# Kernel tuning notes

Hardware: AMD Instinct MI355X
Metric: run time of the kernel (lower is better)

The kernel has to match this reference:

```python
import jax, jax.numpy as jnp
import numpy as np

DIM = 1024
N_HEADS = 16
N_KV = 4
HEAD_DIM = 64
HIDDEN = 2048
N_EXP = 8
TOP_K = 2
B, T = 2, 1024
EPS = 1e-6


def rmsnorm(x, w):
    rms = jnp.sqrt(jnp.mean(x * x, axis=-1, keepdims=True) + EPS)
    return w * x / rms


def apply_rope(x, cos, sin):
    # x: [B, H, T, D]; cos/sin: [T, D//2]
    Tn = x.shape[2]
    c = cos[None, None, :Tn, :]
    s = sin[None, None, :Tn, :]
    xe = x[..., 0::2]
    xo = x[..., 1::2]
    re = xe * c - xo * s
    ro = xe * s + xo * c
    return jnp.stack([re, ro], axis=-1).reshape(x.shape)


def setup_inputs() -> dict:
    key = jax.random.key(0)
    ks = jax.random.split(key, 12)
    sd = DIM ** -0.5
    x = jax.random.normal(ks[0], (B, T, DIM), dtype=jnp.float32)
    # RoPE tables
    half = HEAD_DIM // 2
    inv_freq = 1.0 / (10000.0 ** (np.arange(0, half, dtype=np.float32) / half))
    pos = np.arange(T, dtype=np.float32)
    ang = np.outer(pos, inv_freq)
    cos = jnp.asarray(np.cos(ang), dtype=jnp.float32)
    sin = jnp.asarray(np.sin(ang), dtype=jnp.float32)
    return {
        "x": x,
        "cos": cos,
        "sin": sin,
        "norm_attn_w": jnp.ones((DIM,), jnp.float32),
        "wq": jax.random.normal(ks[1], (N_HEADS * HEAD_DIM, DIM), jnp.float32) * sd,
        "wk": jax.random.normal(ks[2], (N_KV * HEAD_DIM, DIM), jnp.float32) * sd,
        "wv": jax.random.normal(ks[3], (N_KV * HEAD_DIM, DIM), jnp.float32) * sd,
        "wo": jax.random.normal(ks[4], (DIM, N_HEADS * HEAD_DIM), jnp.float32) * sd,
        "norm_ffn_w": jnp.ones((DIM,), jnp.float32),
        "router_w": jax.random.normal(ks[5], (N_EXP, DIM), jnp.float32) * sd,
        "router_b": jnp.zeros((N_EXP,), jnp.float32),
        "w_gate": jax.random.normal(ks[6], (N_EXP, HIDDEN, DIM), jnp.float32) * sd,
        "w_up": jax.random.normal(ks[7], (N_EXP, HIDDEN, DIM), jnp.float32) * sd,
        "w_down": jax.random.normal(ks[8], (N_EXP, DIM, HIDDEN), jnp.float32) * (HIDDEN ** -0.5),
    }


def attention(x, cos, sin, wq, wk, wv, wo):
    Bn, Tn, _ = x.shape
    q = (x @ wq.T).reshape(Bn, Tn, N_HEADS, HEAD_DIM).transpose(0, 2, 1, 3)
    k = (x @ wk.T).reshape(Bn, Tn, N_KV, HEAD_DIM).transpose(0, 2, 1, 3)
    v = (x @ wv.T).reshape(Bn, Tn, N_KV, HEAD_DIM).transpose(0, 2, 1, 3)
    q = apply_rope(q, cos, sin)
    k = apply_rope(k, cos, sin)
    rep = N_HEADS // N_KV
    k = jnp.repeat(k, rep, axis=1)
    v = jnp.repeat(v, rep, axis=1)
    scale = HEAD_DIM ** -0.5
    scores = jnp.einsum("bhqd,bhkd->bhqk", q, k) * scale
    causal = jnp.triu(jnp.ones((Tn, Tn), dtype=bool), k=1)
    scores = jnp.where(causal[None, None], -jnp.inf, scores)
    attn = jax.nn.softmax(scores, axis=-1)
    out = jnp.einsum("bhqk,bhkd->bhqd", attn, v)
    out = out.transpose(0, 2, 1, 3).reshape(Bn, Tn, N_HEADS * HEAD_DIM)
    return out @ wo.T


def moe(x, router_w, router_b, w_gate, w_up, w_down):
    Bn, Tn, D = x.shape
    flat = x.reshape(-1, D)  # [N, D]
    N = flat.shape[0]
    logits = flat @ router_w.T + router_b
    probs = jax.nn.softmax(logits, axis=-1)
    top_vals, top_idx = jax.lax.top_k(probs, TOP_K)
    top_vals = top_vals / (jnp.sum(top_vals, axis=-1, keepdims=True) + 1e-9)
    # combine weights [N, E]
    comb = jnp.zeros((N, N_EXP), flat.dtype).at[jnp.arange(N)[:, None], top_idx].add(top_vals)
    g = jnp.einsum("nd,ehd->enh", flat, w_gate)
    u = jnp.einsum("nd,ehd->enh", flat, w_up)
    h = jax.nn.silu(g) * u
    eo = jnp.einsum("enh,edh->end", h, w_down)  # [E, N, D]
    out = jnp.einsum("ne,end->nd", comb, eo)
    return out.reshape(Bn, Tn, D)


def reference(x, cos, sin, norm_attn_w, wq, wk, wv, wo, norm_ffn_w, router_w, router_b, w_gate, w_up, w_down):
    x = x + attention(rmsnorm(x, norm_attn_w), cos, sin, wq, wk, wv, wo)
    x = x + moe(rmsnorm(x, norm_ffn_w), router_w, router_b, w_gate, w_up, w_down)
    return x
```

## Files before the change

### kernel.cpp

```cpp
#include <hip/hip_runtime.h>
#include <math.h>

#define N_TOK   2048
#define SEQ     1024
#define DIMM    1024
#define NH      16
#define NKV     4
#define HD      64
#define HID     2048
#define NEXP    8
#define QKVW    1536

typedef __attribute__((ext_vector_type(4))) float f32x4;
typedef __attribute__((ext_vector_type(8))) short s16x8;
typedef unsigned short u16;

__device__ __forceinline__ u16 f2bf(float f) {
    union { float f; unsigned u; } v; v.f = f;
    unsigned r = v.u + 0x7fffu + ((v.u >> 16) & 1u);
    return (u16)(r >> 16);
}
__device__ __forceinline__ float bf2f(u16 h) {
    union { unsigned u; float f; } v; v.u = ((unsigned)h) << 16;
    return v.f;
}

__device__ __forceinline__ f32x4 mfma16(s16x8 a, s16x8 b, f32x4 c) {
    return __builtin_amdgcn_mfma_f32_16x16x32_bf16(a, b, c, 0, 0, 0);
}

__device__ __forceinline__ int lds_byte(int row, int byte_in_row, int swz_key) {
    return row * 128 + (byte_in_row ^ ((swz_key & 7) << 4));
}

__device__ __forceinline__ s16x8 ldfrag(const char* base, int row, int ks, int lane) {
    int b = lds_byte(row, ks * 64 + ((lane >> 4) * 16), row);
    return *(const s16x8*)(base + b);
}

__device__ __forceinline__ void gload16(const void* g, void* l) {
    __builtin_amdgcn_global_load_lds(
        (const __attribute__((address_space(1))) void*)g,
        (__attribute__((address_space(3))) void*)l, 16, 0, 0);
}

__global__ __launch_bounds__(256) void cvt_all(const float* __restrict__ wq,
    const float* __restrict__ wk, const float* __restrict__ wv, const float* __restrict__ wo,
    u16* __restrict__ hi, u16* __restrict__ lo,
    const float* __restrict__ a, const float* __restrict__ b, const float* __restrict__ c,
    u16* __restrict__ oa, u16* __restrict__ ob, u16* __restrict__ oc)
{
    if (blockIdx.x < 1024) {
        int i = blockIdx.x * 256 + threadIdx.x;
        int stride = 1024 * 256;
        for (; i < 655360; i += stride) {
            const float* in; int j;
            if (i < 262144)      { in = wq; j = i; }
            else if (i < 327680) { in = wk; j = i - 262144; }
            else if (i < 393216) { in = wv; j = i - 327680; }
            else                 { in = wo; j = i - 393216; }
            f32x4 v = __builtin_nontemporal_load((const f32x4*)in + j);
            ushort4 h, l;
            h.x = f2bf(v[0]); h.y = f2bf(v[1]); h.z = f2bf(v[2]); h.w = f2bf(v[3]);
            l.x = f2bf(v[0] - bf2f(h.x)); l.y = f2bf(v[1] - bf2f(h.y));
            l.z = f2bf(v[2] - bf2f(h.z)); l.w = f2bf(v[3] - bf2f(h.w));
            reinterpret_cast<ushort4*>(hi)[i] = h;
            reinterpret_cast<ushort4*>(lo)[i] = l;
        }
    } else {
        const int n4 = 4 << 20;
        int i = ((blockIdx.x - 1024) * 256 + threadIdx.x) * 2;
        int stride = 3072 * 256 * 2;
        for (; i < 3 * n4; i += stride) {
            int seg = i >> 22, j = i & (n4 - 1);
            const f32x4* in = (const f32x4*)((seg == 0) ? a : (seg == 1) ? b : c);
            ushort4* out = (ushort4*)((seg == 0) ? oa : (seg == 1) ? ob : oc);
            f32x4 v0 = __builtin_nontemporal_load(in + j);
            f32x4 v1 = __builtin_nontemporal_load(in + j + 1);
            ushort4 o0, o1;
            o0.x = f2bf(v0[0]); o0.y = f2bf(v0[1]); o0.z = f2bf(v0[2]); o0.w = f2bf(v0[3]);
            o1.x = f2bf(v1[0]); o1.y = f2bf(v1[1]); o1.z = f2bf(v1[2]); o1.w = f2bf(v1[3]);
            out[j] = o0;
            out[j + 1] = o1;
        }
    }
}

__global__ __launch_bounds__(256) void rmsnorm_split(const float* __restrict__ x,
    const float* __restrict__ w, u16* __restrict__ oh, u16* __restrict__ ol)
{
    int row = blockIdx.x;
    const float4* xr = reinterpret_cast<const float4*>(x + (size_t)row * DIMM);
    const float4* wr = reinterpret_cast<const float4*>(w);
    float4 v = xr[threadIdx.x];
    float ss = v.x*v.x + v.y*v.y + v.z*v.z + v.w*v.w;
#pragma unroll
    for (int off = 32; off; off >>= 1) ss += __shfl_xor(ss, off);
    __shared__ float red[4];
    int wid = threadIdx.x >> 6, lane = threadIdx.x & 63;
    if (lane == 0) red[wid] = ss;
    __syncthreads();
    float tot = red[0] + red[1] + red[2] + red[3];
    float inv = rsqrtf(tot * (1.0f/DIMM) + 1e-6f);
    float4 ww = wr[threadIdx.x];
    float4 o;
    o.x = ww.x * v.x * inv;
    o.y = ww.y * v.y * inv;
    o.z = ww.z * v.z * inv;
    o.w = ww.w * v.w * inv;
    ushort4 h, l;
    h.x = f2bf(o.x); h.y = f2bf(o.y); h.z = f2bf(o.z); h.w = f2bf(o.w);
    l.x = f2bf(o.x - bf2f(h.x)); l.y = f2bf(o.y - bf2f(h.y));
    l.z = f2bf(o.z - bf2f(h.z)); l.w = f2bf(o.w - bf2f(h.w));
    reinterpret_cast<ushort4*>(oh + (size_t)row * DIMM)[threadIdx.x] = h;
    reinterpret_cast<ushort4*>(ol + (size_t)row * DIMM)[threadIdx.x] = l;
}

__global__ __launch_bounds__(256) void rmsnorm_router(const float* __restrict__ x,
    const float* __restrict__ w, const float* __restrict__ rw, const float* __restrict__ rb,
    u16* __restrict__ outb, float* __restrict__ logits)
{
    int row = blockIdx.x;
    int tid = threadIdx.x;
    int wid = tid >> 6, lane = tid & 63;
    const float4* xr = reinterpret_cast<const float4*>(x + (size_t)row * DIMM);
    const float4* wr = reinterpret_cast<const float4*>(w);
    float4 v = xr[tid];
    float ss = v.x*v.x + v.y*v.y + v.z*v.z + v.w*v.w;
#pragma unroll
    for (int off = 32; off; off >>= 1) ss += __shfl_xor(ss, off);
    __shared__ float red[4];
    __shared__ float lred[4][NEXP];
    if (lane == 0) red[wid] = ss;
    __syncthreads();
    float tot = red[0] + red[1] + red[2] + red[3];
    float inv = rsqrtf(tot * (1.0f/DIMM) + 1e-6f);
    float4 ww = wr[tid];
    float4 o;
    o.x = ww.x * v.x * inv;
    o.y = ww.y * v.y * inv;
    o.z = ww.z * v.z * inv;
    o.w = ww.w * v.w * inv;
    ushort4 ob;
    ob.x = f2bf(o.x); ob.y = f2bf(o.y); ob.z = f2bf(o.z); ob.w = f2bf(o.w);
    reinterpret_cast<ushort4*>(outb + (size_t)row * DIMM)[tid] = ob;
    float acc[NEXP];
#pragma unroll
    for (int e = 0; e < NEXP; e++) {
        float4 r4 = reinterpret_cast<const float4*>(rw + (size_t)e * DIMM)[tid];
        acc[e] = o.x * r4.x + o.y * r4.y + o.z * r4.z + o.w * r4.w;
    }
#pragma unroll
    for (int e = 0; e < NEXP; e++) {
        float p = acc[e];
#pragma unroll
        for (int off = 32; off; off >>= 1) p += __shfl_xor(p, off);
        acc[e] = p;
    }
    if (lane == 0)
#pragma unroll
        for (int e = 0; e < NEXP; e++) lred[wid][e] = acc[e];
    __syncthreads();
    if (tid < NEXP)
        logits[(size_t)row * NEXP + tid] =
            lred[0][tid] + lred[1][tid] + lred[2][tid] + lred[3][tid] + rb[tid];
}

__global__ __launch_bounds__(256) void top2_kernel(const float* __restrict__ logits,
    int* __restrict__ top_idx, float* __restrict__ top_w)
{
    int n = blockIdx.x * 256 + threadIdx.x;
    if (n >= N_TOK) return;
    float lg[NEXP];
#pragma unroll
    for (int e = 0; e < NEXP; e++) lg[e] = logits[(size_t)n * NEXP + e];
    float m = lg[0];
#pragma unroll
    for (int e = 1; e < NEXP; e++) m = fmaxf(m, lg[e]);
    float pe[NEXP], s = 0.f;
#pragma unroll
    for (int e = 0; e < NEXP; e++) { pe[e] = __expf(lg[e] - m); s += pe[e]; }
    int i1 = 0; float v1 = pe[0];
#pragma unroll
    for (int e = 1; e < NEXP; e++) if (pe[e] > v1) { v1 = pe[e]; i1 = e; }
    int i2 = -1; float v2 = -1.f;
#pragma unroll
    for (int e = 0; e < NEXP; e++) if (e != i1 && pe[e] > v2) { v2 = pe[e]; i2 = e; }
    v1 /= s; v2 /= s;
    float den = v1 + v2 + 1e-9f;
    top_idx[2 * n] = i1; top_idx[2 * n + 1] = i2;
    top_w[2 * n] = v1 / den; top_w[2 * n + 1] = v2 / den;
}

__global__ __launch_bounds__(256) void route_build(const int* __restrict__ top_idx,
    const float* __restrict__ top_w, int* __restrict__ counts, int* __restrict__ offs,
    int* __restrict__ assign_token, float* __restrict__ assign_w)
{
    __shared__ int lcnt[NEXP], loff[NEXP], lpos[NEXP];
    int tid = threadIdx.x;
    if (tid < NEXP) { lcnt[tid] = 0; lpos[tid] = 0; }
    __syncthreads();
    for (int i = tid; i < 2 * N_TOK; i += 256)
        atomicAdd(&lcnt[top_idx[i]], 1);
    __syncthreads();
    if (tid == 0) {
        int s = 0;
        for (int e = 0; e < NEXP; e++) { loff[e] = s; s += lcnt[e]; }
    }
    __syncthreads();
    if (tid < NEXP) { counts[tid] = lcnt[tid]; offs[tid] = loff[tid]; }
    for (int i = tid; i < 2 * N_TOK; i += 256) {
        int e = top_idx[i];
        int p = atomicAdd(&lpos[e], 1);
        int r = loff[e] + p;
        assign_token[r] = i >> 1;
        assign_w[r] = top_w[i];
    }
}

__global__ __launch_bounds__(256) void gemm_bs(const u16* __restrict__ Ah_,
    const u16* __restrict__ Al_, const u16* __restrict__ Bh_, const u16* __restrict__ Bl_,
    float* __restrict__ C, const float* __restrict__ R, int M, int N, int K, int ldc)
{
    __shared__ __align__(16) u16 Ah[128 * 64], Al[128 * 64];
    __shared__ __align__(16) u16 Bh[64 * 64],  Bl[64 * 64];
    int tid = threadIdx.x;
    int m0 = blockIdx.y * 128, n0 = blockIdx.x * 64;
    int lane = tid & 63, wv = tid >> 6;
    int wm = wv >> 1, wn = wv & 1;
    int sr = lane >> 3, sc = lane & 7;

    f32x4 acc[4][2];
#pragma unroll
    for (int i = 0; i < 4; i++)
#pragma unroll
        for (int j = 0; j < 2; j++) acc[i][j] = f32x4{0.f, 0.f, 0.f, 0.f};

    const int NT = K >> 6;
    int bid = blockIdx.x + gridDim.x * blockIdx.y;
    int ph = (bid * 5) & (NT - 1);

    for (int tt = 0; tt < NT; ++tt) {
        int k0 = ((tt + ph) & (NT - 1)) << 6;
#pragma unroll
        for (int i = 0; i < 4; i++) {
            int row = wv * 32 + i * 8 + sr;
            int c = sc ^ (row & 7);
            size_t g = (size_t)(m0 + row) * K + k0 + c * 8;
            gload16(Ah_ + g, (void*)(Ah + (wv * 4 + i) * 512));
            gload16(Al_ + g, (void*)(Al + (wv * 4 + i) * 512));
        }
#pragma unroll
        for (int i = 0; i < 2; i++) {
            int row = wv * 16 + i * 8 + sr;
            int c = sc ^ (row & 7);
            size_t g = (size_t)(n0 + row) * K + k0 + c * 8;
            gload16(Bh_ + g, (void*)(Bh + (wv * 2 + i) * 512));
            gload16(Bl_ + g, (void*)(Bl + (wv * 2 + i) * 512));
        }
        __syncthreads();
#pragma unroll
        for (int ks = 0; ks < 2; ++ks) {
            s16x8 afh[4], afl[4], bfh[2], bfl[2];
#pragma unroll
            for (int mi = 0; mi < 4; mi++) {
                int row = wm * 64 + mi * 16 + (lane & 15);
                afh[mi] = ldfrag((const char*)Ah, row, ks, lane);
                afl[mi] = ldfrag((const char*)Al, row, ks, lane);
            }
#pragma unroll
            for (int nj = 0; nj < 2; nj++) {
                int row = wn * 32 + nj * 16 + (lane & 15);
                bfh[nj] = ldfrag((const char*)Bh, row, ks, lane);
                bfl[nj] = ldfrag((const char*)Bl, row, ks, lane);
            }
#pragma unroll
            for (int mi = 0; mi < 4; mi++)
#pragma unroll
                for (int nj = 0; nj < 2; nj++) {
                    acc[mi][nj] = mfma16(afl[mi], bfh[nj], acc[mi][nj]);
                    acc[mi][nj] = mfma16(afh[mi], bfl[nj], acc[mi][nj]);
                    acc[mi][nj] = mfma16(afh[mi], bfh[nj], acc[mi][nj]);
                }
        }
        __syncthreads();
    }
#pragma unroll
    for (int mi = 0; mi < 4; mi++)
#pragma unroll
        for (int nj = 0; nj < 2; nj++)
#pragma unroll
            for (int r = 0; r < 4; r++) {
                int m = m0 + wm * 64 + mi * 16 + (lane >> 4) * 4 + r;
                int n = n0 + wn * 32 + nj * 16 + (lane & 15);
                float v = acc[mi][nj][r];
                if (R) v += R[(size_t)m * ldc + n];
                C[(size_t)m * ldc + n] = v;
            }
}

__global__ __launch_bounds__(256) void rope_both(const float* __restrict__ qkvb,
    const float* __restrict__ cs, const float* __restrict__ sn,
    u16* __restrict__ qsh, u16* __restrict__ qsl,
    u16* __restrict__ ksh, u16* __restrict__ ksl)
{
    int gid = blockIdx.x * 256 + threadIdx.x;
    const int QTOT = N_TOK * NH * 32;
    const int KTOT = N_TOK * NKV * 32;
    int nheads, base_col, out_w;
    u16 *oh, *ol;
    if (gid < QTOT) {
        nheads = NH; base_col = 0; out_w = NH * HD; oh = qsh; ol = qsl;
    } else {
        gid -= QTOT;
        if (gid >= KTOT) return;
        nheads = NKV; base_col = 1024; out_w = NKV * HD; oh = ksh; ol = ksl;
    }
    int i = gid & 31;
    int h = (gid >> 5) % nheads;
    int n = gid / (32 * nheads);
    int t = n & (SEQ - 1);
    const float* p = qkvb + (size_t)n * QKVW + base_col + h * HD + 2 * i;
    float xe = p[0], xo = p[1];
    float c = cs[t * 32 + i], s = sn[t * 32 + i];
    float re = xe * c - xo * s;
    float ro = xe * s + xo * c;
    size_t o = (size_t)n * out_w + h * HD + 2 * i;
    u16 reh = f2bf(re), roh = f2bf(ro);
    oh[o] = reh;     oh[o + 1] = roh;
    ol[o] = f2bf(re - bf2f(reh));
    ol[o + 1] = f2bf(ro - bf2f(roh));
}

__global__ __launch_bounds__(256) void transpose_v_split(const float* __restrict__ qkvb,
    u16* __restrict__ vth, u16* __restrict__ vtl)
{
    __shared__ float t[64][65];
    int bx = blockIdx.x;
    int by = blockIdx.y;
    int tid = threadIdx.x;
    int c4 = tid & 15, r0 = tid >> 4;
#pragma unroll
    for (int i = 0; i < 4; i++) {
        int row = r0 + i * 16;
        float4 vv = *(const float4*)(qkvb + (size_t)(bx * 64 + row) * QKVW + 1280 + by * 64 + c4 * 4);
        t[c4 * 4 + 0][row] = vv.x;
        t[c4 * 4 + 1][row] = vv.y;
        t[c4 * 4 + 2][row] = vv.z;
        t[c4 * 4 + 3][row] = vv.w;
    }
    __syncthreads();
#pragma unroll
    for (int i = 0; i < 4; i++) {
        int drow = r0 + i * 16;
        ushort4 hh, ll;
        float a = t[drow][c4 * 4 + 0], b = t[drow][c4 * 4 + 1];
        float c = t[drow][c4 * 4 + 2], d = t[drow][c4 * 4 + 3];
        hh.x = f2bf(a); hh.y = f2bf(b); hh.z = f2bf(c); hh.w = f2bf(d);
        ll.x = f2bf(a - bf2f(hh.x)); ll.y = f2bf(b - bf2f(hh.y));
        ll.z = f2bf(c - bf2f(hh.z)); ll.w = f2bf(d - bf2f(hh.w));
        size_t o = ((size_t)(by * 64 + drow) * N_TOK + bx * 64 + c4 * 4) >> 2;
        reinterpret_cast<ushort4*>(vth)[o] = hh;
        reinterpret_cast<ushort4*>(vtl)[o] = ll;
    }
}

__global__ __launch_bounds__(256) void attn_mfma(const u16* __restrict__ qsh,
    const u16* __restrict__ qsl, const u16* __restrict__ ksh, const u16* __restrict__ ksl,
    const u16* __restrict__ vth, const u16* __restrict__ vtl,
    u16* __restrict__ outh, u16* __restrict__ outl)
{
    int b = blockIdx.z, h = blockIdx.y;
    int qt = (gridDim.x - 1) - blockIdx.x;
    int kvh = h >> 2;
    int tid = threadIdx.x;
    int lane = tid & 63, wv = tid >> 6;
    int q0 = qt * 64;
    int sr = lane >> 3, sc = lane & 7;

    __shared__ __align__(16) u16 Qh[64 * 64], Ql[64 * 64];
    __shared__ __align__(16) u16 Kh[64 * 64], Kl[64 * 64];
    __shared__ __align__(16) u16 Vh[64 * 64], Vl[64 * 64];
    __shared__ __align__(16) char Ph[4][16 * 128], Pl[4][16 * 128];

#pragma unroll
    for (int i = 0; i < 2; i++) {
        int row = wv * 16 + i * 8 + sr;
        int c = sc ^ (row & 7);
        size_t g = (size_t)(b * SEQ + q0 + row) * (NH * HD) + h * HD + c * 8;
        gload16(qsh + g, (void*)(Qh + (wv * 2 + i) * 512));
        gload16(qsl + g, (void*)(Ql + (wv * 2 + i) * 512));
    }
    __syncthreads();

    s16x8 aQh[2], aQl[2];
#pragma unroll
    for (int ks = 0; ks < 2; ks++) {
        aQh[ks] = ldfrag((const char*)Qh, wv * 16 + (lane & 15), ks, lane);
        aQl[ks] = ldfrag((const char*)Ql, wv * 16 + (lane & 15), ks, lane);
    }

    float m_run[4], l_run[4];
    f32x4 acc_o[4];
#pragma unroll
    for (int r = 0; r < 4; r++) { m_run[r] = -1e30f; l_run[r] = 0.f; }
#pragma unroll
    for (int nj = 0; nj < 4; nj++) acc_o[nj] = f32x4{0.f, 0.f, 0.f, 0.f};

    for (int kt = 0; kt <= qt; kt++) {
        int kbase = kt * 64;
        __syncthreads();
#pragma unroll
        for (int i = 0; i < 2; i++) {
            int row = wv * 16 + i * 8 + sr;
            int c = sc ^ (row & 7);
            size_t gk = (size_t)(b * SEQ + kbase + row) * (NKV * HD) + kvh * HD + c * 8;
            size_t gv = (size_t)(kvh * HD + row) * N_TOK + b * SEQ + kbase + c * 8;
            gload16(ksh + gk, (void*)(Kh + (wv * 2 + i) * 512));
            gload16(ksl + gk, (void*)(Kl + (wv * 2 + i) * 512));
            gload16(vth + gv, (void*)(Vh + (wv * 2 + i) * 512));
            gload16(vtl + gv, (void*)(Vl + (wv * 2 + i) * 512));
        }
        __syncthreads();

        f32x4 sacc[4];
#pragma unroll
        for (int nj = 0; nj < 4; nj++) sacc[nj] = f32x4{0.f, 0.f, 0.f, 0.f};
#pragma unroll
        for (int ks = 0; ks < 2; ks++) {
#pragma unroll
            for (int nj = 0; nj < 4; nj++) {
                s16x8 bKh = ldfrag((const char*)Kh, nj * 16 + (lane & 15), ks, lane);
                s16x8 bKl = ldfrag((const char*)Kl, nj * 16 + (lane & 15), ks, lane);
                sacc[nj] = mfma16(aQl[ks], bKh, sacc[nj]);
                sacc[nj] = mfma16(aQh[ks], bKl, sacc[nj]);
                sacc[nj] = mfma16(aQh[ks], bKh, sacc[nj]);
            }
        }

        float sv[4][4];
#pragma unroll
        for (int nj = 0; nj < 4; nj++)
#pragma unroll
            for (int r = 0; r < 4; r++) {
                float s = sacc[nj][r] * 0.125f;
                if (kt == qt) {
                    int row_loc = wv * 16 + (lane >> 4) * 4 + r;
                    int col_loc = nj * 16 + (lane & 15);
                    if (col_loc > row_loc) s = -1e30f;
                }
                sv[nj][r] = s;
            }

        float p[4][4];
#pragma unroll
        for (int r = 0; r < 4; r++) {
            float mx = fmaxf(fmaxf(sv[0][r], sv[1][r]), fmaxf(sv[2][r], sv[3][r]));
            mx = fmaxf(mx, __shfl_xor(mx, 1));
            mx = fmaxf(mx, __shfl_xor(mx, 2));
            mx = fmaxf(mx, __shfl_xor(mx, 4));
            mx = fmaxf(mx, __shfl_xor(mx, 8));
            float m_new = fmaxf(m_run[r], mx);
            float corr = __expf(m_run[r] - m_new);
            float ps = 0.f;
#pragma unroll
            for (int nj = 0; nj < 4; nj++) {
                float pv = __expf(sv[nj][r] - m_new);
                p[nj][r] = pv;
                ps += pv;
            }
            ps += __shfl_xor(ps, 1);
            ps += __shfl_xor(ps, 2);
            ps += __shfl_xor(ps, 4);
            ps += __shfl_xor(ps, 8);
            l_run[r] = l_run[r] * corr + ps;
            m_run[r] = m_new;
#pragma unroll
            for (int nj = 0; nj < 4; nj++) acc_o[nj][r] *= corr;
        }

        char* phb = Ph[wv];
        char* plb = Pl[wv];
#pragma unroll
        for (int nj = 0; nj < 4; nj++)
#pragma unroll
            for (int r = 0; r < 4; r++) {
                int row = (lane >> 4) * 4 + r;
                int col = nj * 16 + (lane & 15);
                u16 hh = f2bf(p[nj][r]);
                u16 ll = f2bf(p[nj][r] - bf2f(hh));
                int byte = lds_byte(row, col * 2, row);
                *(u16*)(phb + byte) = hh;
                *(u16*)(plb + byte) = ll;
            }

#pragma unroll
        for (int ks = 0; ks < 2; ks++) {
            s16x8 aPh = ldfrag(phb, lane & 15, ks, lane);
            s16x8 aPl = ldfrag(plb, lane & 15, ks, lane);
#pragma unroll
            for (int nj = 0; nj < 4; nj++) {
                s16x8 bVh = ldfrag((const char*)Vh, nj * 16 + (lane & 15), ks, lane);
                s16x8 bVl = ldfrag((const char*)Vl, nj * 16 + (lane & 15), ks, lane);
                acc_o[nj] = mfma16(aPl, bVh, acc_o[nj]);
                acc_o[nj] = mfma16(aPh, bVl, acc_o[nj]);
                acc_o[nj] = mfma16(aPh, bVh, acc_o[nj]);
            }
        }
    }

#pragma unroll
    for (int r = 0; r < 4; r++) {
        int row_glob = q0 + wv * 16 + (lane >> 4) * 4 + r;
        float inv = 1.f / l_run[r];
#pragma unroll
        for (int nj = 0; nj < 4; nj++) {
            int dv = nj * 16 + (lane & 15);
            size_t idx = (size_t)(b * SEQ + row_glob) * (NH * HD) + h * HD + dv;
            float v = acc_o[nj][r] * inv;
            u16 hh = f2bf(v);
            outh[idx] = hh;
            outl[idx] = f2bf(v - bf2f(hh));
        }
    }
}

__global__ __launch_bounds__(256) void moe_gateup2(const u16* __restrict__ xb,
    const u16* __restrict__ wgb, const u16* __restrict__ wub,
    const int* __restrict__ assign_token, const int* __restrict__ offs,
    const int* __restrict__ counts, u16* __restrict__ hbufb)
{
    int e = blockIdx.z;
    int cnt = counts[e];
    int t0 = blockIdx.y * 128;
    if (t0 >= cnt) return;
    int base = offs[e];
    int h0 = blockIdx.x * 64;
    __shared__ __align__(16) u16 As[128 * 64];
    __shared__ __align__(16) u16 Gs[64 * 64];
    __shared__ __align__(16) u16 Us[64 * 64];
    __shared__ int toks[128];
    int tid = threadIdx.x;
    if (tid < 128) {
        int a = t0 + tid;
        toks[tid] = (a < cnt) ? assign_token[base + a] : 0;
    }
    __syncthreads();
    int lane = tid & 63, wv = tid >> 6;
    int wm = wv >> 1, wn = wv & 1;
    int sr = lane >> 3, sc = lane & 7;

    int tokr[4];
#pragma unroll
    for (int i = 0; i < 4; i++) tokr[i] = toks[wv * 32 + i * 8 + sr];

    const u16* wge = wgb + (size_t)e * HID * DIMM;
    const u16* wue = wub + (size_t)e * HID * DIMM;

    f32x4 accg[4][2], accu[4][2];
#pragma unroll
    for (int i = 0; i < 4; i++)
#pragma unroll
        for (int j = 0; j < 2; j++) { accg[i][j] = f32x4{0,0,0,0}; accu[i][j] = f32x4{0,0,0,0}; }

    const int NT = DIMM / 64;
    int bid = blockIdx.x + gridDim.x * (blockIdx.y + gridDim.y * blockIdx.z);
    int ph = (bid * 5) & (NT - 1);

    for (int tt = 0; tt < NT; ++tt) {
        int k0 = ((tt + ph) & (NT - 1)) << 6;
#pragma unroll
        for (int i = 0; i < 4; i++) {
            int row = wv * 32 + i * 8 + sr;
            int c = sc ^ (row & 7);
            gload16(xb + (size_t)tokr[i] * DIMM + k0 + c * 8, (void*)(As + (wv * 4 + i) * 512));
        }
#pragma unroll
        for (int i = 0; i < 2; i++) {
            int row = wv * 16 + i * 8 + sr;
            int c = sc ^ (row & 7);
            gload16(wge + (size_t)(h0 + row) * DIMM + k0 + c * 8, (void*)(Gs + (wv * 2 + i) * 512));
            gload16(wue + (size_t)(h0 + row) * DIMM + k0 + c * 8, (void*)(Us + (wv * 2 + i) * 512));
        }
        __syncthreads();
#pragma unroll
        for (int ks = 0; ks < 2; ++ks) {
            s16x8 af[4], gf[2], uf[2];
#pragma unroll
            for (int mi = 0; mi < 4; mi++)
                af[mi] = ldfrag((const char*)As, wm * 64 + mi * 16 + (lane & 15), ks, lane);
#pragma unroll
            for (int nj = 0; nj < 2; nj++) {
                int row = wn * 32 + nj * 16 + (lane & 15);
                gf[nj] = ldfrag((const char*)Gs, row, ks, lane);
                uf[nj] = ldfrag((const char*)Us, row, ks, lane);
            }
#pragma unroll
            for (int mi = 0; mi < 4; mi++)
#pragma unroll
                for (int nj = 0; nj < 2; nj++) {
                    accg[mi][nj] = mfma16(af[mi], gf[nj], accg[mi][nj]);
                    accu[mi][nj] = mfma16(af[mi], uf[nj], accu[mi][nj]);
                }
        }
        __syncthreads();
    }
#pragma unroll
    for (int mi = 0; mi < 4; mi++)
#pragma unroll
        for (int nj = 0; nj < 2; nj++)
#pragma unroll
            for (int r = 0; r < 4; r++) {
                int row = wm * 64 + mi * 16 + (lane >> 4) * 4 + r;
                if (t0 + row < cnt) {
                    int col = wn * 32 + nj * 16 + (lane & 15);
                    float g = accg[mi][nj][r], u = accu[mi][nj][r];
                    float hh = (g / (1.f + __expf(-g))) * u;
                    hbufb[(size_t)(base + t0 + row) * HID + h0 + col] = f2bf(hh);
                }
            }
}

__global__ __launch_bounds__(256) void moe_down2(const u16* __restrict__ hbufb,
    const u16* __restrict__ wdb, const int* __restrict__ assign_token,
    const float* __restrict__ assign_w, const int* __restrict__ offs,
    const int* __restrict__ counts, float* __restrict__ out)
{
    int e = blockIdx.z;
    int cnt = counts[e];
    int t0 = blockIdx.y * 128;
    if (t0 >= cnt) return;
    int base = offs[e];
    int d0 = blockIdx.x * 128;
    __shared__ __align__(16) u16 As[128 * 64];
    __shared__ __align__(16) u16 Bs[128 * 64];
    __shared__ int toks[128];
    __shared__ float rw_[128];
    int tid = threadIdx.x;
    if (tid < 128) {
        int a = t0 + tid;
        toks[tid] = (a < cnt) ? assign_token[base + a] : 0;
        rw_[tid] = (a < cnt) ? assign_w[base + a] : 0.f;
    }
    __syncthreads();
    int lane = tid & 63, wv = tid >> 6;
    int wm = wv >> 1, wn = wv & 1;
    int sr = lane >> 3, sc = lane & 7;

    const u16* wde = wdb + (size_t)e * DIMM * HID;

    f32x4 acc[4][4];
#pragma unroll
    for (int i = 0; i < 4; i++)
#pragma unroll
        for (int j = 0; j < 4; j++) acc[i][j] = f32x4{0,0,0,0};

    const int NT = HID / 64;
    int bid = blockIdx.x + gridDim.x * (blockIdx.y + gridDim.y * blockIdx.z);
    int ph = (bid * 5) & (NT - 1);

    for (int tt = 0; tt < NT; ++tt) {
        int k0 = ((tt + ph) & (NT - 1)) << 6;
#pragma unroll
        for (int i = 0; i < 4; i++) {
            int row = wv * 32 + i * 8 + sr;
            int c = sc ^ (row & 7);
            gload16(hbufb + (size_t)(base + t0 + row) * HID + k0 + c * 8, (void*)(As + (wv * 4 + i) * 512));
            gload16(wde + (size_t)(d0 + row) * HID + k0 + c * 8, (void*)(Bs + (wv * 4 + i) * 512));
        }
        __syncthreads();
#pragma unroll
        for (int ks = 0; ks < 2; ++ks) {
            s16x8 af[4];
#pragma unroll
            for (int mi = 0; mi < 4; mi++)
                af[mi] = ldfrag((const char*)As, wm * 64 + mi * 16 + (lane & 15), ks, lane);
#pragma unroll
            for (int nj = 0; nj < 4; nj++) {
                s16x8 bf = ldfrag((const char*)Bs, wn * 64 + nj * 16 + (lane & 15), ks, lane);
#pragma unroll
                for (int mi = 0; mi < 4; mi++)
                    acc[mi][nj] = mfma16(af[mi], bf, acc[mi][nj]);
            }
        }
        __syncthreads();
    }
#pragma unroll
    for (int mi = 0; mi < 4; mi++)
#pragma unroll
        for (int r = 0; r < 4; r++) {
            int row = wm * 64 + mi * 16 + (lane >> 4) * 4 + r;
            if (t0 + row < cnt) {
                int tok = toks[row];
                float w = rw_[row];
#pragma unroll
                for (int nj = 0; nj < 4; nj++) {
                    int col = d0 + wn * 64 + nj * 16 + (lane & 15);
                    atomicAdd(&out[(size_t)tok * DIMM + col], acc[mi][nj][r] * w);
                }
            }
        }
}

extern "C" void kernel_launch(void* const* d_in, const int* in_sizes, int n_in,
                              void* d_out, int out_size, void* d_ws, size_t ws_size,
                              hipStream_t stream)
{
    const float* x      = (const float*)d_in[0];
    const float* cs     = (const float*)d_in[1];
    const float* sn     = (const float*)d_in[2];
    const float* w_na   = (const float*)d_in[3];
    const float* wq     = (const float*)d_in[4];
    const float* wk     = (const float*)d_in[5];
    const float* wv     = (const float*)d_in[6];
    const float* wo     = (const float*)d_in[7];
    const float* w_nf   = (const float*)d_in[8];
    const float* rw     = (const float*)d_in[9];
    const float* rb     = (const float*)d_in[10];
    const float* wg     = (const float*)d_in[11];
    const float* wu     = (const float*)d_in[12];
    const float* wd     = (const float*)d_in[13];
    float* out = (float*)d_out;

    const size_t F = 1024 * 1024;
    float* wsf = (float*)d_ws;

    float* qkvb = wsf;
    float* tail = wsf + 3 * F;
    u16* qsh    = (u16*)(wsf + 3 * F + F / 2);
    u16* qsl    = (u16*)(wsf + 4 * F + F / 2);
    u16* ksh    = (u16*)(wsf + 5 * F + F / 2);
    u16* ksl    = (u16*)(wsf + 5 * F + 3 * F / 4);
    u16* vth    = (u16*)(wsf + 6 * F);
    u16* vtl    = (u16*)(wsf + 6 * F + F / 4);
    u16* xn2b   = (u16*)(wsf + 6 * F + F / 2);
    u16* hbufb  = (u16*)(wsf + 7 * F + F / 2);
    u16* xnh    = (u16*)(wsf + 7 * F + F / 2);
    u16* xnl    = (u16*)(wsf + 8 * F + F / 2);
    u16* attnh  = (u16*)(wsf + 9 * F + F / 2);
    u16* attnl  = (u16*)(wsf + 10 * F + F / 2);
    u16* wgb    = (u16*)(wsf + 11 * F + F / 2);
    u16* wub    = (u16*)(wsf + 19 * F + F / 2);
    u16* wdb    = (u16*)(wsf + 27 * F + F / 2);
    u16* wqkvoh = (u16*)(wsf + 35 * F + F / 2);
    u16* wqkvol = (u16*)(wsf + 36 * F + 3 * F / 4);

    int*   top_idx      = (int*)tail;
    float* top_w        = tail + 4096;
    int*   counts       = (int*)(tail + 8192);
    int*   offs         = (int*)(tail + 8192) + 8;
    int*   assign_token = (int*)(tail + 8192) + 32;
    float* assign_w     = tail + 8192 + 32 + 4096;
    float* logits       = tail + 8192 + 32 + 8192;

    cvt_all<<<4096, 256, 0, stream>>>(wq, wk, wv, wo, wqkvoh, wqkvol,
                                      wg, wu, wd, wgb, wub, wdb);
    rmsnorm_split<<<N_TOK, 256, 0, stream>>>(x, w_na, xnh, xnl);
    gemm_bs<<<dim3(QKVW / 64, 16), 256, 0, stream>>>(xnh, xnl, wqkvoh, wqkvol,
                                                     qkvb, nullptr, N_TOK, QKVW, DIMM, QKVW);
    rope_both<<<(N_TOK * (NH + NKV) * 32 + 255) / 256, 256, 0, stream>>>(qkvb, cs, sn, qsh, qsl, ksh, ksl);
    transpose_v_split<<<dim3(N_TOK / 64, (NKV * HD) / 64), 256, 0, stream>>>(qkvb, vth, vtl);
    attn_mfma<<<dim3(SEQ / 64, NH, 2), 256, 0, stream>>>(qsh, qsl, ksh, ksl, vth, vtl, attnh, attnl);
    gemm_bs<<<dim3(DIMM / 64, 16), 256, 0, stream>>>(attnh, attnl,
                                                     wqkvoh + (size_t)1536 * 1024, wqkvol + (size_t)1536 * 1024,
                                                     out, x, N_TOK, DIMM, NH * HD, DIMM);
    rmsnorm_router<<<N_TOK, 256, 0, stream>>>(out, w_nf, rw, rb, xn2b, logits);
    top2_kernel<<<N_TOK / 256, 256, 0, stream>>>(logits, top_idx, top_w);
    route_build<<<1, 256, 0, stream>>>(top_idx, top_w, counts, offs, assign_token, assign_w);
    moe_gateup2<<<dim3(HID / 64, 16, NEXP), 256, 0, stream>>>(xn2b, wgb, wub, assign_token, offs, counts, hbufb);
    moe_down2<<<dim3(DIMM / 128, 16, NEXP), 256, 0, stream>>>(hbufb, wdb, assign_token, assign_w, offs, counts, out);
}
```

Baseline: 332.4 us.

## Merge small kernels and overlap MoE weight conversion with attention

```diff
diff --git a/kernel.cpp b/kernel.cpp
--- a/kernel.cpp
+++ b/kernel.cpp
@@ -44,11 +44,11 @@
         (__attribute__((address_space(3))) void*)l, 16, 0, 0);
 }
 
-__global__ __launch_bounds__(256) void cvt_all(const float* __restrict__ wq,
+__global__ __launch_bounds__(256) void prep1(const float* __restrict__ wq,
     const float* __restrict__ wk, const float* __restrict__ wv, const float* __restrict__ wo,
     u16* __restrict__ hi, u16* __restrict__ lo,
-    const float* __restrict__ a, const float* __restrict__ b, const float* __restrict__ c,
-    u16* __restrict__ oa, u16* __restrict__ ob, u16* __restrict__ oc)
+    const float* __restrict__ x, const float* __restrict__ w_na,
+    u16* __restrict__ oh, u16* __restrict__ ol)
 {
     if (blockIdx.x < 1024) {
         int i = blockIdx.x * 256 + threadIdx.x;
@@ -68,57 +68,37 @@
             reinterpret_cast<ushort4*>(lo)[i] = l;
         }
     } else {
-        const int n4 = 4 << 20;
-        int i = ((blockIdx.x - 1024) * 256 + threadIdx.x) * 2;
-        int stride = 3072 * 256 * 2;
-        for (; i < 3 * n4; i += stride) {
-            int seg = i >> 22, j = i & (n4 - 1);
-            const f32x4* in = (const f32x4*)((seg == 0) ? a : (seg == 1) ? b : c);
-            ushort4* out = (ushort4*)((seg == 0) ? oa : (seg == 1) ? ob : oc);
-            f32x4 v0 = __builtin_nontemporal_load(in + j);
-            f32x4 v1 = __builtin_nontemporal_load(in + j + 1);
-            ushort4 o0, o1;
-            o0.x = f2bf(v0[0]); o0.y = f2bf(v0[1]); o0.z = f2bf(v0[2]); o0.w = f2bf(v0[3]);
-            o1.x = f2bf(v1[0]); o1.y = f2bf(v1[1]); o1.z = f2bf(v1[2]); o1.w = f2bf(v1[3]);
-            out[j] = o0;
-            out[j + 1] = o1;
-        }
-    }
-}
-
-__global__ __launch_bounds__(256) void rmsnorm_split(const float* __restrict__ x,
-    const float* __restrict__ w, u16* __restrict__ oh, u16* __restrict__ ol)
-{
-    int row = blockIdx.x;
-    const float4* xr = reinterpret_cast<const float4*>(x + (size_t)row * DIMM);
-    const float4* wr = reinterpret_cast<const float4*>(w);
-    float4 v = xr[threadIdx.x];
-    float ss = v.x*v.x + v.y*v.y + v.z*v.z + v.w*v.w;
-#pragma unroll
-    for (int off = 32; off; off >>= 1) ss += __shfl_xor(ss, off);
-    __shared__ float red[4];
-    int wid = threadIdx.x >> 6, lane = threadIdx.x & 63;
-    if (lane == 0) red[wid] = ss;
-    __syncthreads();
-    float tot = red[0] + red[1] + red[2] + red[3];
-    float inv = rsqrtf(tot * (1.0f/DIMM) + 1e-6f);
-    float4 ww = wr[threadIdx.x];
-    float4 o;
-    o.x = ww.x * v.x * inv;
-    o.y = ww.y * v.y * inv;
-    o.z = ww.z * v.z * inv;
-    o.w = ww.w * v.w * inv;
-    ushort4 h, l;
-    h.x = f2bf(o.x); h.y = f2bf(o.y); h.z = f2bf(o.z); h.w = f2bf(o.w);
-    l.x = f2bf(o.x - bf2f(h.x)); l.y = f2bf(o.y - bf2f(h.y));
-    l.z = f2bf(o.z - bf2f(h.z)); l.w = f2bf(o.w - bf2f(h.w));
-    reinterpret_cast<ushort4*>(oh + (size_t)row * DIMM)[threadIdx.x] = h;
-    reinterpret_cast<ushort4*>(ol + (size_t)row * DIMM)[threadIdx.x] = l;
+        int row = blockIdx.x - 1024;
+        const float4* xr = reinterpret_cast<const float4*>(x + (size_t)row * DIMM);
+        const float4* wr = reinterpret_cast<const float4*>(w_na);
+        float4 v = xr[threadIdx.x];
+        float ss = v.x*v.x + v.y*v.y + v.z*v.z + v.w*v.w;
+#pragma unroll
+        for (int off = 32; off; off >>= 1) ss += __shfl_xor(ss, off);
+        __shared__ float red[4];
+        int wid = threadIdx.x >> 6, lane = threadIdx.x & 63;
+        if (lane == 0) red[wid] = ss;
+        __syncthreads();
+        float tot = red[0] + red[1] + red[2] + red[3];
+        float inv = rsqrtf(tot * (1.0f/DIMM) + 1e-6f);
+        float4 ww = wr[threadIdx.x];
+        float4 o;
+        o.x = ww.x * v.x * inv;
+        o.y = ww.y * v.y * inv;
+        o.z = ww.z * v.z * inv;
+        o.w = ww.w * v.w * inv;
+        ushort4 h, l;
+        h.x = f2bf(o.x); h.y = f2bf(o.y); h.z = f2bf(o.z); h.w = f2bf(o.w);
+        l.x = f2bf(o.x - bf2f(h.x)); l.y = f2bf(o.y - bf2f(h.y));
+        l.z = f2bf(o.z - bf2f(h.z)); l.w = f2bf(o.w - bf2f(h.w));
+        reinterpret_cast<ushort4*>(oh + (size_t)row * DIMM)[threadIdx.x] = h;
+        reinterpret_cast<ushort4*>(ol + (size_t)row * DIMM)[threadIdx.x] = l;
+    }
 }
 
 __global__ __launch_bounds__(256) void rmsnorm_router(const float* __restrict__ x,
     const float* __restrict__ w, const float* __restrict__ rw, const float* __restrict__ rb,
-    u16* __restrict__ outb, float* __restrict__ logits)
+    u16* __restrict__ outb, int* __restrict__ top_idx, float* __restrict__ top_w)
 {
     int row = blockIdx.x;
     int tid = threadIdx.x;
@@ -161,35 +141,28 @@
 #pragma unroll
         for (int e = 0; e < NEXP; e++) lred[wid][e] = acc[e];
     __syncthreads();
-    if (tid < NEXP)
-        logits[(size_t)row * NEXP + tid] =
-            lred[0][tid] + lred[1][tid] + lred[2][tid] + lred[3][tid] + rb[tid];
-}
-
-__global__ __launch_bounds__(256) void top2_kernel(const float* __restrict__ logits,
-    int* __restrict__ top_idx, float* __restrict__ top_w)
-{
-    int n = blockIdx.x * 256 + threadIdx.x;
-    if (n >= N_TOK) return;
-    float lg[NEXP];
-#pragma unroll
-    for (int e = 0; e < NEXP; e++) lg[e] = logits[(size_t)n * NEXP + e];
-    float m = lg[0];
-#pragma unroll
-    for (int e = 1; e < NEXP; e++) m = fmaxf(m, lg[e]);
-    float pe[NEXP], s = 0.f;
-#pragma unroll
-    for (int e = 0; e < NEXP; e++) { pe[e] = __expf(lg[e] - m); s += pe[e]; }
-    int i1 = 0; float v1 = pe[0];
-#pragma unroll
-    for (int e = 1; e < NEXP; e++) if (pe[e] > v1) { v1 = pe[e]; i1 = e; }
-    int i2 = -1; float v2 = -1.f;
-#pragma unroll
-    for (int e = 0; e < NEXP; e++) if (e != i1 && pe[e] > v2) { v2 = pe[e]; i2 = e; }
-    v1 /= s; v2 /= s;
-    float den = v1 + v2 + 1e-9f;
-    top_idx[2 * n] = i1; top_idx[2 * n + 1] = i2;
-    top_w[2 * n] = v1 / den; top_w[2 * n + 1] = v2 / den;
+    if (tid == 0) {
+        float lg[NEXP];
+#pragma unroll
+        for (int e = 0; e < NEXP; e++)
+            lg[e] = lred[0][e] + lred[1][e] + lred[2][e] + lred[3][e] + rb[e];
+        float m = lg[0];
+#pragma unroll
+        for (int e = 1; e < NEXP; e++) m = fmaxf(m, lg[e]);
+        float pe[NEXP], s = 0.f;
+#pragma unroll
+        for (int e = 0; e < NEXP; e++) { pe[e] = __expf(lg[e] - m); s += pe[e]; }
+        int i1 = 0; float v1 = pe[0];
+#pragma unroll
+        for (int e = 1; e < NEXP; e++) if (pe[e] > v1) { v1 = pe[e]; i1 = e; }
+        int i2 = -1; float v2 = -1.f;
+#pragma unroll
+        for (int e = 0; e < NEXP; e++) if (e != i1 && pe[e] > v2) { v2 = pe[e]; i2 = e; }
+        v1 /= s; v2 /= s;
+        float den = v1 + v2 + 1e-9f;
+        top_idx[2 * row] = i1; top_idx[2 * row + 1] = i2;
+        top_w[2 * row] = v1 / den; top_w[2 * row + 1] = v2 / den;
+    }
 }
 
 __global__ __launch_bounds__(256) void route_build(const int* __restrict__ top_idx,
@@ -299,79 +272,100 @@
             }
 }
 
-__global__ __launch_bounds__(256) void rope_both(const float* __restrict__ qkvb,
+__global__ __launch_bounds__(256) void prep2(const float* __restrict__ qkvb,
     const float* __restrict__ cs, const float* __restrict__ sn,
     u16* __restrict__ qsh, u16* __restrict__ qsl,
-    u16* __restrict__ ksh, u16* __restrict__ ksl)
-{
-    int gid = blockIdx.x * 256 + threadIdx.x;
-    const int QTOT = N_TOK * NH * 32;
-    const int KTOT = N_TOK * NKV * 32;
-    int nheads, base_col, out_w;
-    u16 *oh, *ol;
-    if (gid < QTOT) {
-        nheads = NH; base_col = 0; out_w = NH * HD; oh = qsh; ol = qsl;
+    u16* __restrict__ ksh, u16* __restrict__ ksl,
+    u16* __restrict__ vth, u16* __restrict__ vtl)
+{
+    const int ROPE_BLOCKS = (N_TOK * (NH + NKV) * 32) / 256;
+    if (blockIdx.x < ROPE_BLOCKS) {
+        int gid = blockIdx.x * 256 + threadIdx.x;
+        const int QTOT = N_TOK * NH * 32;
+        int nheads, base_col, out_w;
+        u16 *oh, *ol;
+        if (gid < QTOT) {
+            nheads = NH; base_col = 0; out_w = NH * HD; oh = qsh; ol = qsl;
+        } else {
+            gid -= QTOT;
+            nheads = NKV; base_col = 1024; out_w = NKV * HD; oh = ksh; ol = ksl;
+        }
+        int i = gid & 31;
+        int h = (gid >> 5) % nheads;
+        int n = gid / (32 * nheads);
+        int t = n & (SEQ - 1);
+        const float* p = qkvb + (size_t)n * QKVW + base_col + h * HD + 2 * i;
+        float xe = p[0], xo = p[1];
+        float c = cs[t * 32 + i], s = sn[t * 32 + i];
+        float re = xe * c - xo * s;
+        float ro = xe * s + xo * c;
+        size_t o = (size_t)n * out_w + h * HD + 2 * i;
+        u16 reh = f2bf(re), roh = f2bf(ro);
+        oh[o] = reh;     oh[o + 1] = roh;
+        ol[o] = f2bf(re - bf2f(reh));
+        ol[o + 1] = f2bf(ro - bf2f(roh));
     } else {
-        gid -= QTOT;
-        if (gid >= KTOT) return;
-        nheads = NKV; base_col = 1024; out_w = NKV * HD; oh = ksh; ol = ksl;
-    }
-    int i = gid & 31;
-    int h = (gid >> 5) % nheads;
-    int n = gid / (32 * nheads);
-    int t = n & (SEQ - 1);
-    const float* p = qkvb + (size_t)n * QKVW + base_col + h * HD + 2 * i;
-    float xe = p[0], xo = p[1];
-    float c = cs[t * 32 + i], s = sn[t * 32 + i];
-    float re = xe * c - xo * s;
-    float ro = xe * s + xo * c;
-    size_t o = (size_t)n * out_w + h * HD + 2 * i;
-    u16 reh = f2bf(re), roh = f2bf(ro);
-    oh[o] = reh;     oh[o + 1] = roh;
-    ol[o] = f2bf(re - bf2f(reh));
-    ol[o + 1] = f2bf(ro - bf2f(roh));
-}
-
-__global__ __launch_bounds__(256) void transpose_v_split(const float* __restrict__ qkvb,
-    u16* __restrict__ vth, u16* __restrict__ vtl)
-{
-    __shared__ float t[64][65];
-    int bx = blockIdx.x;
-    int by = blockIdx.y;
-    int tid = threadIdx.x;
-    int c4 = tid & 15, r0 = tid >> 4;
-#pragma unroll
-    for (int i = 0; i < 4; i++) {
-        int row = r0 + i * 16;
-        float4 vv = *(const float4*)(qkvb + (size_t)(bx * 64 + row) * QKVW + 1280 + by * 64 + c4 * 4);
-        t[c4 * 4 + 0][row] = vv.x;
-        t[c4 * 4 + 1][row] = vv.y;
-        t[c4 * 4 + 2][row] = vv.z;
-        t[c4 * 4 + 3][row] = vv.w;
-    }
-    __syncthreads();
-#pragma unroll
-    for (int i = 0; i < 4; i++) {
-        int drow = r0 + i * 16;
-        ushort4 hh, ll;
-        float a = t[drow][c4 * 4 + 0], b = t[drow][c4 * 4 + 1];
-        float c = t[drow][c4 * 4 + 2], d = t[drow][c4 * 4 + 3];
-        hh.x = f2bf(a); hh.y = f2bf(b); hh.z = f2bf(c); hh.w = f2bf(d);
-        ll.x = f2bf(a - bf2f(hh.x)); ll.y = f2bf(b - bf2f(hh.y));
-        ll.z = f2bf(c - bf2f(hh.z)); ll.w = f2bf(d - bf2f(hh.w));
-        size_t o = ((size_t)(by * 64 + drow) * N_TOK + bx * 64 + c4 * 4) >> 2;
-        reinterpret_cast<ushort4*>(vth)[o] = hh;
-        reinterpret_cast<ushort4*>(vtl)[o] = ll;
-    }
-}
-
-__global__ __launch_bounds__(256) void attn_mfma(const u16* __restrict__ qsh,
+        __shared__ float t[64][65];
+        int r = blockIdx.x - ROPE_BLOCKS;
+        int bx = r & 31;
+        int by = r >> 5;
+        int tid = threadIdx.x;
+        int c4 = tid & 15, r0 = tid >> 4;
+#pragma unroll
+        for (int i = 0; i < 4; i++) {
+            int row = r0 + i * 16;
+            float4 vv = *(const float4*)(qkvb + (size_t)(bx * 64 + row) * QKVW + 1280 + by * 64 + c4 * 4);
+            t[c4 * 4 + 0][row] = vv.x;
+            t[c4 * 4 + 1][row] = vv.y;
+            t[c4 * 4 + 2][row] = vv.z;
+            t[c4 * 4 + 3][row] = vv.w;
+        }
+        __syncthreads();
+#pragma unroll
+        for (int i = 0; i < 4; i++) {
+            int drow = r0 + i * 16;
+            ushort4 hh, ll;
+            float a = t[drow][c4 * 4 + 0], b = t[drow][c4 * 4 + 1];
+            float c = t[drow][c4 * 4 + 2], d = t[drow][c4 * 4 + 3];
+            hh.x = f2bf(a); hh.y = f2bf(b); hh.z = f2bf(c); hh.w = f2bf(d);
+            ll.x = f2bf(a - bf2f(hh.x)); ll.y = f2bf(b - bf2f(hh.y));
+            ll.z = f2bf(c - bf2f(hh.z)); ll.w = f2bf(d - bf2f(hh.w));
+            size_t o = ((size_t)(by * 64 + drow) * N_TOK + bx * 64 + c4 * 4) >> 2;
+            reinterpret_cast<ushort4*>(vth)[o] = hh;
+            reinterpret_cast<ushort4*>(vtl)[o] = ll;
+        }
+    }
+}
+
+__global__ __launch_bounds__(256) void attn_cvt(const u16* __restrict__ qsh,
     const u16* __restrict__ qsl, const u16* __restrict__ ksh, const u16* __restrict__ ksl,
     const u16* __restrict__ vth, const u16* __restrict__ vtl,
-    u16* __restrict__ outh, u16* __restrict__ outl)
-{
-    int b = blockIdx.z, h = blockIdx.y;
-    int qt = (gridDim.x - 1) - blockIdx.x;
+    u16* __restrict__ outh, u16* __restrict__ outl,
+    const float* __restrict__ wg, const float* __restrict__ wu, const float* __restrict__ wd,
+    u16* __restrict__ wgb, u16* __restrict__ wub, u16* __restrict__ wdb)
+{
+    if (blockIdx.x >= 512) {
+        const int n4 = 4 << 20;
+        int i = ((blockIdx.x - 512) * 256 + threadIdx.x) * 2;
+        int stride = 3072 * 256 * 2;
+        for (; i < 3 * n4; i += stride) {
+            int seg = i >> 22, j = i & (n4 - 1);
+            const f32x4* in = (const f32x4*)((seg == 0) ? wg : (seg == 1) ? wu : wd);
+            ushort4* out = (ushort4*)((seg == 0) ? wgb : (seg == 1) ? wub : wdb);
+            f32x4 v0 = __builtin_nontemporal_load(in + j);
+            f32x4 v1 = __builtin_nontemporal_load(in + j + 1);
+            ushort4 o0, o1;
+            o0.x = f2bf(v0[0]); o0.y = f2bf(v0[1]); o0.z = f2bf(v0[2]); o0.w = f2bf(v0[3]);
+            o1.x = f2bf(v1[0]); o1.y = f2bf(v1[1]); o1.z = f2bf(v1[2]); o1.w = f2bf(v1[3]);
+            out[j] = o0;
+            out[j + 1] = o1;
+        }
+        return;
+    }
+    int bi = blockIdx.x;
+    int b = bi >> 8;
+    int h = (bi >> 4) & 15;
+    int qt = 15 - (bi & 15);
     int kvh = h >> 2;
     int tid = threadIdx.x;
     int lane = tid & 63, wv = tid >> 6;
@@ -751,21 +745,17 @@
     int*   offs         = (int*)(tail + 8192) + 8;
     int*   assign_token = (int*)(tail + 8192) + 32;
     float* assign_w     = tail + 8192 + 32 + 4096;
-    float* logits       = tail + 8192 + 32 + 8192;
-
-    cvt_all<<<4096, 256, 0, stream>>>(wq, wk, wv, wo, wqkvoh, wqkvol,
-                                      wg, wu, wd, wgb, wub, wdb);
-    rmsnorm_split<<<N_TOK, 256, 0, stream>>>(x, w_na, xnh, xnl);
+
+    prep1<<<3072, 256, 0, stream>>>(wq, wk, wv, wo, wqkvoh, wqkvol, x, w_na, xnh, xnl);
     gemm_bs<<<dim3(QKVW / 64, 16), 256, 0, stream>>>(xnh, xnl, wqkvoh, wqkvol,
                                                      qkvb, nullptr, N_TOK, QKVW, DIMM, QKVW);
-    rope_both<<<(N_TOK * (NH + NKV) * 32 + 255) / 256, 256, 0, stream>>>(qkvb, cs, sn, qsh, qsl, ksh, ksl);
-    transpose_v_split<<<dim3(N_TOK / 64, (NKV * HD) / 64), 256, 0, stream>>>(qkvb, vth, vtl);
-    attn_mfma<<<dim3(SEQ / 64, NH, 2), 256, 0, stream>>>(qsh, qsl, ksh, ksl, vth, vtl, attnh, attnl);
+    prep2<<<5248, 256, 0, stream>>>(qkvb, cs, sn, qsh, qsl, ksh, ksl, vth, vtl);
+    attn_cvt<<<3584, 256, 0, stream>>>(qsh, qsl, ksh, ksl, vth, vtl, attnh, attnl,
+                                       wg, wu, wd, wgb, wub, wdb);
     gemm_bs<<<dim3(DIMM / 64, 16), 256, 0, stream>>>(attnh, attnl,
                                                      wqkvoh + (size_t)1536 * 1024, wqkvol + (size_t)1536 * 1024,
                                                      out, x, N_TOK, DIMM, NH * HD, DIMM);
-    rmsnorm_router<<<N_TOK, 256, 0, stream>>>(out, w_nf, rw, rb, xn2b, logits);
-    top2_kernel<<<N_TOK / 256, 256, 0, stream>>>(logits, top_idx, top_w);
+    rmsnorm_router<<<N_TOK, 256, 0, stream>>>(out, w_nf, rw, rb, xn2b, top_idx, top_w);
     route_build<<<1, 256, 0, stream>>>(top_idx, top_w, counts, offs, assign_token, assign_w);
     moe_gateup2<<<dim3(HID / 64, 16, NEXP), 256, 0, stream>>>(xn2b, wgb, wub, assign_token, offs, counts, hbufb);
     moe_down2<<<dim3(DIMM / 128, 16, NEXP), 256, 0, stream>>>(hbufb, wdb, assign_token, assign_w, offs, counts, out);
```

New measurement: 321.5 us. 1.03x faster.
